# Kernel tuning notes

Measured on AMD Instinct MI355X. Metric: run time of the kernel, lower is better.

The kernel has to match this reference:

```python
import jax, jax.numpy as jnp
import numpy as np

N_NODES = 50000
N_EDGES = 800000
N_GRAPHS = 512
D_NODE = 64
D_EDGE = 32
Z_DIM = 2 * D_NODE + D_EDGE  # 160


def setup_inputs() -> dict:
    key = jax.random.key(0)
    ks = jax.random.split(key, 12)
    inp = {
        'x': jax.random.normal(ks[0], (N_NODES, D_NODE), dtype=jnp.float32),
        'edge_index': jax.random.randint(ks[1], (2, N_EDGES), 0, N_NODES, dtype=jnp.int64),
        'edge_attr': jax.random.uniform(ks[2], (N_EDGES, D_EDGE), dtype=jnp.float32),
        'batch': jnp.sort(jax.random.randint(ks[3], (N_NODES,), 0, N_GRAPHS, dtype=jnp.int64)),
        'Wf1': jax.random.normal(ks[4], (Z_DIM, D_NODE), dtype=jnp.float32) * 0.05,
        'bf1': jnp.zeros((D_NODE,), dtype=jnp.float32),
        'Ws1': jax.random.normal(ks[5], (Z_DIM, D_NODE), dtype=jnp.float32) * 0.05,
        'bs1': jnp.zeros((D_NODE,), dtype=jnp.float32),
        'Wf2': jax.random.normal(ks[6], (Z_DIM, D_NODE), dtype=jnp.float32) * 0.05,
        'bf2': jnp.zeros((D_NODE,), dtype=jnp.float32),
        'Ws2': jax.random.normal(ks[7], (Z_DIM, D_NODE), dtype=jnp.float32) * 0.05,
        'bs2': jnp.zeros((D_NODE,), dtype=jnp.float32),
        'W_out': jax.random.normal(ks[8], (D_NODE, 1), dtype=jnp.float32) * 0.05,
        'b_out': jnp.zeros((1,), dtype=jnp.float32),
    }
    return inp


def _cgconv(x, edge_index, edge_attr, Wf, bf, Ws, bs):
    # PyG CGConv: out_i = x_i + sum_{j in N(i)} sigmoid(lin_f(z_ij)) * softplus(lin_s(z_ij))
    # with z_ij = [x_i, x_j, e_ij]; source_to_target flow: j=edge_index[0], i=edge_index[1]
    src, dst = edge_index[0], edge_index[1]
    z = jnp.concatenate([x[dst], x[src], edge_attr], axis=-1)  # [E, 2d+dim]
    msg = jax.nn.sigmoid(z @ Wf + bf) * jax.nn.softplus(z @ Ws + bs)  # [E, d]
    aggr = jax.ops.segment_sum(msg, dst, num_segments=x.shape[0])
    return x + aggr


def reference(x, edge_index, edge_attr, batch, Wf1, bf1, Ws1, bs1, Wf2, bf2, Ws2, bs2, W_out, b_out):
    h = _cgconv(x, edge_index, edge_attr, Wf1, bf1, Ws1, bs1)
    h = _cgconv(h, edge_index, edge_attr, Wf2, bf2, Ws2, bs2)
    pooled = jax.ops.segment_sum(h, batch, num_segments=N_GRAPHS)  # global_add_pool [G, d]
    out = pooled @ W_out + b_out  # [G, 1]
    return out
```

## Files before the change

### kernel.cpp

```cpp
#include <hip/hip_runtime.h>
#include <math.h>

#define N_NODES 50000
#define N_EDGES 800000
#define N_GRAPHS 512
#define D 64
#define DE 32
#define NB_SCAN 196
#define NSTR 136
#define NB_SCAT 3125
#define NB_NT 1563
#define NB_FUSED 4689


typedef __attribute__((ext_vector_type(8))) short short8;
typedef __attribute__((ext_vector_type(4))) float floatx4;
union Frag { short8 s; unsigned u[4]; };
union U4   { uint4 v; unsigned u[4]; };

__device__ inline unsigned pk_bf16(float lo, float hi) {
    unsigned a = __float_as_uint(lo);
    unsigned b = __float_as_uint(hi);
    a = (a + 0x7FFFu + ((a >> 16) & 1u)) >> 16;
    b = (b + 0x7FFFu + ((b >> 16) & 1u)) >> 16;
    return a | (b << 16);
}
__device__ inline unsigned short bf16_1(float v) {
    unsigned a = __float_as_uint(v);
    return (unsigned short)((a + 0x7FFFu + ((a >> 16) & 1u)) >> 16);
}
__device__ inline float upk(unsigned u16) { return __uint_as_float(u16 << 16); }

__global__ __launch_bounds__(256) void hist_kernel(
    const int* __restrict__ ei, int* __restrict__ deg, int* __restrict__ rank)
{
    int e = blockIdx.x * 256 + threadIdx.x;
    rank[e] = atomicAdd(&deg[ei[N_EDGES + e]], 1);
}

__global__ __launch_bounds__(256) void scan1(
    const int* __restrict__ deg, int* __restrict__ off, int* __restrict__ tsum)
{
    __shared__ int s[256];
    int i = blockIdx.x * 256 + threadIdx.x;
    s[threadIdx.x] = (i < N_NODES) ? deg[i] : 0;
    __syncthreads();
    if (threadIdx.x == 0) {
        int run = 0;
        for (int k = 0; k < 256; ++k) { int t = s[k]; s[k] = run; run += t; }
        tsum[blockIdx.x] = run;
    }
    __syncthreads();
    if (i < N_NODES) off[i] = s[threadIdx.x];
}

__global__ __launch_bounds__(256) void scan2(int* __restrict__ tsum)
{
    __shared__ int s[256];
    int i = threadIdx.x;
    s[i] = (i < NB_SCAN) ? tsum[i] : 0;
    __syncthreads();
    if (i == 0) {
        int run = 0;
        for (int k = 0; k < NB_SCAN; ++k) { int t = s[k]; s[k] = run; run += t; }
    }
    __syncthreads();
    if (i < NB_SCAN) tsum[i] = s[i];
}

__global__ __launch_bounds__(256) void scan3(
    int* __restrict__ off, const int* __restrict__ tsum)
{
    int i = blockIdx.x * 256 + threadIdx.x;
    if (i < N_NODES) off[i] += tsum[blockIdx.x];
    if (i == N_NODES) off[i] = N_EDGES;
}

__global__ __launch_bounds__(256) void pack_W(
    const float* __restrict__ Wf1, const float* __restrict__ Ws1,
    const float* __restrict__ Wf2, const float* __restrict__ Ws2,
    uint4* __restrict__ WpkNT, uint4* __restrict__ WpkE)
{
    const int layer = blockIdx.y;
    const float* Wf = layer ? Wf2 : Wf1;
    const float* Ws = layer ? Ws2 : Ws1;
    const int i = blockIdx.x * 256 + threadIdx.x;
    if (i < 1024) {
        const int p    = i >> 9;
        const int cbi  = (i >> 6) & 7;
        const int l    = i & 63;
        const int n16  = l & 15, quad = l >> 4, kc = quad * 8;
        const int col  = cbi * 16 + n16;
        const int j    = col >> 1;
        const float* Wsel = (col & 1) ? Ws : Wf;
        const int rbase = p * 64;
        U4 b0, b1;
#pragma unroll
        for (int pp = 0; pp < 4; ++pp) {
            b0.u[pp] = pk_bf16(Wsel[(rbase + kc + 2 * pp) * 64 + j],
                               Wsel[(rbase + kc + 2 * pp + 1) * 64 + j]);
            b1.u[pp] = pk_bf16(Wsel[(rbase + 32 + kc + 2 * pp) * 64 + j],
                               Wsel[(rbase + 32 + kc + 2 * pp + 1) * 64 + j]);
        }
        uint4* o = WpkNT + ((size_t)layer * 1024 + i) * 2;
        o[0] = b0.v; o[1] = b1.v;
    } else if (i < 1280) {
        const int k  = i - 1024;
        const int jb = k >> 6;
        const int l  = k & 63;
        const int n16 = l & 15, quad = l >> 4, c0 = quad * 8;
        const int j = jb * 16 + n16;
        U4 bf_, bs_;
#pragma unroll
        for (int pp = 0; pp < 4; ++pp) {
            bf_.u[pp] = pk_bf16(Wf[(128 + c0 + 2 * pp) * 64 + j],
                                Wf[(128 + c0 + 2 * pp + 1) * 64 + j]);
            bs_.u[pp] = pk_bf16(Ws[(128 + c0 + 2 * pp) * 64 + j],
                                Ws[(128 + c0 + 2 * pp + 1) * 64 + j]);
        }
        uint4* o = WpkE + ((size_t)layer * 256 + k) * 2;
        o[0] = bf_.v; o[1] = bs_.v;
    }
}

__global__ __launch_bounds__(256) void fused_scatter_nt(
    const int* __restrict__ ei, const int* __restrict__ off,
    const int* __restrict__ rank, const float* __restrict__ ea,
    unsigned short* __restrict__ eaS, int2* __restrict__ sd_sorted,
    const float* __restrict__ H,
    const float* __restrict__ bf, const float* __restrict__ bs,
    const uint4* __restrict__ Wpk,
    unsigned short* __restrict__ Tdst, unsigned short* __restrict__ Tsrc,
    float* __restrict__ hinit)
{
    __shared__ unsigned short lt[4][16 * NSTR];
    const int k = blockIdx.x;

    if ((k % 3) != 2) {
        const int sid = k - (k / 3);
        if (sid >= NB_SCAT) return;
        int e = sid * 256 + threadIdx.x;
        int s = ei[e];
        int d = ei[N_EDGES + e];
        int pos = off[d] + rank[e];
        sd_sorted[pos] = make_int2(s, d);

        const float4* src4 = (const float4*)(ea + (size_t)e * 32);
        uint4* dst16 = (uint4*)(eaS + (size_t)pos * 32);
#pragma unroll
        for (int q = 0; q < 2; ++q) {
            float4 v0 = src4[4 * q + 0];
            float4 v1 = src4[4 * q + 1];
            float4 v2 = src4[4 * q + 2];
            float4 v3 = src4[4 * q + 3];
            uint4 o0;
            o0.x = pk_bf16(v0.x, v0.y); o0.y = pk_bf16(v0.z, v0.w);
            o0.z = pk_bf16(v1.x, v1.y); o0.w = pk_bf16(v1.z, v1.w);
            uint4 o1;
            o1.x = pk_bf16(v2.x, v2.y); o1.y = pk_bf16(v2.z, v2.w);
            o1.z = pk_bf16(v3.x, v3.y); o1.w = pk_bf16(v3.z, v3.w);
            dst16[2 * q + 0] = o0;
            dst16[2 * q + 1] = o1;
        }
        return;
    }

    const int lane = threadIdx.x & 63;
    const int wid  = threadIdx.x >> 6;
    const int n16  = lane & 15;
    const int quad = lane >> 4;
    const int kc   = quad * 8;
    unsigned short* L = lt[wid];

    const int gid = (k / 3) * 4 + wid;
    const int NW  = (N_NODES / 16) * 2;
    if (gid >= NW) return;
    const int ntile = gid >> 1;
    const int part  = gid & 1;
    unsigned short* Tout = part ? Tsrc : Tdst;

    const float* hrow = H + (size_t)(ntile * 16 + n16) * D;
    float4 q0 = *(const float4*)(hrow + kc);
    float4 q1 = *(const float4*)(hrow + kc + 4);
    float4 q2 = *(const float4*)(hrow + 32 + kc);
    float4 q3 = *(const float4*)(hrow + 32 + kc + 4);
    Frag a0, a1;
    a0.u[0] = pk_bf16(q0.x, q0.y); a0.u[1] = pk_bf16(q0.z, q0.w);
    a0.u[2] = pk_bf16(q1.x, q1.y); a0.u[3] = pk_bf16(q1.z, q1.w);
    a1.u[0] = pk_bf16(q2.x, q2.y); a1.u[1] = pk_bf16(q2.z, q2.w);
    a1.u[2] = pk_bf16(q3.x, q3.y); a1.u[3] = pk_bf16(q3.z, q3.w);

    if (part == 0) {
        float4* hp = (float4*)(hinit + (size_t)(ntile * 16 + n16) * D);
        hp[quad * 2]     = q0;
        hp[quad * 2 + 1] = q1;
        hp[8 + quad * 2] = q2;
        hp[9 + quad * 2] = q3;
    }

#pragma unroll
    for (int cbi = 0; cbi < 8; ++cbi) {
        const int col   = cbi * 16 + n16;
        const int sflag = col & 1;
        const int j     = col >> 1;

        Frag b0, b1;
        {
            const uint4* bp = Wpk + ((size_t)(part * 512 + cbi * 64 + lane)) * 2;
            *(uint4*)&b0 = bp[0];
            *(uint4*)&b1 = bp[1];
        }
        float bias = 0.0f;
        if (part == 0) bias = sflag ? bs[j] : bf[j];

        floatx4 acc = {bias, bias, bias, bias};
        acc = __builtin_amdgcn_mfma_f32_16x16x32_bf16(a0.s, b0.s, acc, 0, 0, 0);
        acc = __builtin_amdgcn_mfma_f32_16x16x32_bf16(a1.s, b1.s, acc, 0, 0, 0);

#pragma unroll
        for (int r = 0; r < 4; ++r)
            L[(quad * 4 + r) * NSTR + col] = bf16_1(acc[r]);
    }

#pragma unroll
    for (int it = 0; it < 4; ++it) {
        const int node_l = it * 4 + quad;
        const int c8     = n16 * 8;
        uint4 v = *(const uint4*)(L + node_l * NSTR + c8);
        *(uint4*)(Tout + (size_t)(ntile * 16 + node_l) * 128 + c8) = v;
    }
}

__global__ __launch_bounds__(256) void node_transform_mfma(
    const float* __restrict__ H,
    const float* __restrict__ bf,
    const float* __restrict__ bs,
    const uint4* __restrict__ Wpk,
    unsigned short* __restrict__ Tdst,
    unsigned short* __restrict__ Tsrc,
    float* __restrict__ hinit)
{
    __shared__ unsigned short lt[4][16 * NSTR];
    const int lane = threadIdx.x & 63;
    const int wid  = threadIdx.x >> 6;
    const int n16  = lane & 15;
    const int quad = lane >> 4;
    const int kc   = quad * 8;
    unsigned short* L = lt[wid];

    const int gid = blockIdx.x * 4 + wid;
    const int NW  = (N_NODES / 16) * 2;
    if (gid >= NW) return;
    const int ntile = gid >> 1;
    const int part  = gid & 1;
    unsigned short* Tout = part ? Tsrc : Tdst;

    const float* hrow = H + (size_t)(ntile * 16 + n16) * D;
    float4 q0 = *(const float4*)(hrow + kc);
    float4 q1 = *(const float4*)(hrow + kc + 4);
    float4 q2 = *(const float4*)(hrow + 32 + kc);
    float4 q3 = *(const float4*)(hrow + 32 + kc + 4);
    Frag a0, a1;
    a0.u[0] = pk_bf16(q0.x, q0.y); a0.u[1] = pk_bf16(q0.z, q0.w);
    a0.u[2] = pk_bf16(q1.x, q1.y); a0.u[3] = pk_bf16(q1.z, q1.w);
    a1.u[0] = pk_bf16(q2.x, q2.y); a1.u[1] = pk_bf16(q2.z, q2.w);
    a1.u[2] = pk_bf16(q3.x, q3.y); a1.u[3] = pk_bf16(q3.z, q3.w);

    if (part == 0) {
        float4* hp = (float4*)(hinit + (size_t)(ntile * 16 + n16) * D);
        hp[quad * 2]     = q0;
        hp[quad * 2 + 1] = q1;
        hp[8 + quad * 2] = q2;
        hp[9 + quad * 2] = q3;
    }

#pragma unroll
    for (int cbi = 0; cbi < 8; ++cbi) {
        const int col   = cbi * 16 + n16;
        const int sflag = col & 1;
        const int j     = col >> 1;

        Frag b0, b1;
        {
            const uint4* bp = Wpk + ((size_t)(part * 512 + cbi * 64 + lane)) * 2;
            *(uint4*)&b0 = bp[0];
            *(uint4*)&b1 = bp[1];
        }
        float bias = 0.0f;
        if (part == 0) bias = sflag ? bs[j] : bf[j];

        floatx4 acc = {bias, bias, bias, bias};
        acc = __builtin_amdgcn_mfma_f32_16x16x32_bf16(a0.s, b0.s, acc, 0, 0, 0);
        acc = __builtin_amdgcn_mfma_f32_16x16x32_bf16(a1.s, b1.s, acc, 0, 0, 0);

#pragma unroll
        for (int r = 0; r < 4; ++r)
            L[(quad * 4 + r) * NSTR + col] = bf16_1(acc[r]);
    }

#pragma unroll
    for (int it = 0; it < 4; ++it) {
        const int node_l = it * 4 + quad;
        const int c8     = n16 * 8;
        uint4 v = *(const uint4*)(L + node_l * NSTR + c8);
        *(uint4*)(Tout + (size_t)(ntile * 16 + node_l) * 128 + c8) = v;
    }
}

__global__ __launch_bounds__(256) void edge_message_mfma(
    const unsigned short* __restrict__ Tdst,
    const unsigned short* __restrict__ Tsrc,
    const unsigned short* __restrict__ eaS,
    const int2* __restrict__ sd_sorted,
    const uint4* __restrict__ WpkE,
    float* __restrict__ hout)
{
    const int lane = threadIdx.x & 63;
    const int wid  = threadIdx.x >> 6;
    const int n16  = lane & 15;
    const int quad = lane >> 4;
    const int c0   = quad * 8;

    Frag bfr[4], bsr[4];
#pragma unroll
    for (int jb = 0; jb < 4; ++jb) {
        *(uint4*)&bfr[jb] = WpkE[((size_t)(jb * 64 + lane)) * 2 + 0];
        *(uint4*)&bsr[jb] = WpkE[((size_t)(jb * 64 + lane)) * 2 + 1];
    }

    const int nwg = gridDim.x;
    const int xcd = blockIdx.x & 7;
    const int idx = blockIdx.x >> 3;
    const int q   = nwg >> 3, rr = nwg & 7;
    const int sb  = (xcd < rr ? xcd * (q + 1) : rr * (q + 1) + (xcd - rr) * q) + idx;
    const int w   = sb * 4 + wid;
    const int base = w * 64;

    const floatx4 zero = {0.0f, 0.0f, 0.0f, 0.0f};

    const int4* sdp4 = (const int4*)(sd_sorted + base + quad * 16);
    int4 sdq[8];
#pragma unroll
    for (int i = 0; i < 8; ++i) sdq[i] = sdp4[i];

#define SV(e) ((((e) & 1) != 0) ? sdq[(e) >> 1].z : sdq[(e) >> 1].x)
#define DV(e) ((((e) & 1) != 0) ? sdq[(e) >> 1].w : sdq[(e) >> 1].y)

    const unsigned short* aptr =
        eaS + (size_t)(base + (n16 >> 2) * 16 + (n16 & 3)) * 32 + c0;
    Frag af;
    af.s = *(const short8*)aptr;

    unsigned sbuf[2][4][4];
#pragma unroll
    for (int r = 0; r < 4; ++r) {
        const unsigned* srow = (const unsigned*)(Tsrc + (size_t)SV(r) * 128);
        sbuf[0][r][0] = srow[n16];
        sbuf[0][r][1] = srow[16 + n16];
        sbuf[0][r][2] = srow[32 + n16];
        sbuf[0][r][3] = srow[48 + n16];
    }

    int cur_d = -1;
    unsigned dr0 = 0, dr1 = 0, dr2 = 0, dr3 = 0;
    float acc0 = 0.f, acc1 = 0.f, acc2 = 0.f, acc3 = 0.f;

#pragma unroll
    for (int tt = 0; tt < 4; ++tt) {
        const int cb = tt & 1, nb = cb ^ 1;
        if (tt < 3) {
#pragma unroll
            for (int r = 0; r < 4; ++r) {
                const unsigned* srow =
                    (const unsigned*)(Tsrc + (size_t)SV(4 * (tt + 1) + r) * 128);
                sbuf[nb][r][0] = srow[n16];
                sbuf[nb][r][1] = srow[16 + n16];
                sbuf[nb][r][2] = srow[32 + n16];
                sbuf[nb][r][3] = srow[48 + n16];
            }
        }

        floatx4 accf[4], accs[4];
#pragma unroll
        for (int jb = 0; jb < 4; ++jb) {
            accf[jb] = __builtin_amdgcn_mfma_f32_16x16x32_bf16(af.s, bfr[jb].s, zero, 0, 0, 0);
            accs[jb] = __builtin_amdgcn_mfma_f32_16x16x32_bf16(af.s, bsr[jb].s, zero, 0, 0, 0);
        }
        if (tt < 3) af.s = *(const short8*)(aptr + (tt + 1) * 128);

#pragma unroll
        for (int r = 0; r < 4; ++r) {
            const int dv = DV(4 * tt + r);
            if (dv != cur_d) {
                if (cur_d >= 0) {
                    float* hp = hout + (size_t)cur_d * D + n16;
                    atomicAdd(hp +  0, acc0);
                    atomicAdd(hp + 16, acc1);
                    atomicAdd(hp + 32, acc2);
                    atomicAdd(hp + 48, acc3);
                }
                cur_d = dv;
                const unsigned* drow = (const unsigned*)(Tdst + (size_t)dv * 128);
                dr0 = drow[n16];
                dr1 = drow[16 + n16];
                dr2 = drow[32 + n16];
                dr3 = drow[48 + n16];
                acc0 = acc1 = acc2 = acc3 = 0.f;
            }
#pragma unroll
            for (int jb = 0; jb < 4; ++jb) {
                unsigned d2 = (jb == 0) ? dr0 : (jb == 1) ? dr1 : (jb == 2) ? dr2 : dr3;
                unsigned sv = sbuf[cb][r][jb];
                float vf = accf[jb][r] + upk(d2 & 0xFFFFu) + upk(sv & 0xFFFFu);
                float vs = accs[jb][r] + upk(d2 >> 16) + upk(sv >> 16);
                float sig = __builtin_amdgcn_rcpf(1.0f + __expf(-vf));
                float spl = fmaxf(vs, 0.0f) + __logf(1.0f + __expf(-fabsf(vs)));
                float msg = sig * spl;
                if      (jb == 0) acc0 += msg;
                else if (jb == 1) acc1 += msg;
                else if (jb == 2) acc2 += msg;
                else              acc3 += msg;
            }
        }
    }
#undef SV
#undef DV
    {
        float* hp = hout + (size_t)cur_d * D + n16;
        atomicAdd(hp +  0, acc0);
        atomicAdd(hp + 16, acc1);
        atomicAdd(hp + 32, acc2);
        atomicAdd(hp + 48, acc3);
    }
}

__global__ __launch_bounds__(256) void pool_kernel(
    const float* __restrict__ h,
    const int* __restrict__ batch,
    float* __restrict__ pooled)
{
    const int lane = threadIdx.x & 63;
    const int wid  = threadIdx.x >> 6;
    const int w = blockIdx.x * 4 + wid;
    const int n0 = w * 16;
    if (n0 >= N_NODES) return;
    const int nend = (n0 + 16 < N_NODES) ? (n0 + 16) : N_NODES;

    int cur = batch[n0];
    float acc = 0.0f;
    for (int n = n0; n < nend; ++n) {
        int b = batch[n];
        float v = h[(size_t)n * D + lane];
        if (b != cur) {
            atomicAdd(&pooled[(size_t)cur * D + lane], acc);
            cur = b; acc = v;
        } else {
            acc += v;
        }
    }
    atomicAdd(&pooled[(size_t)cur * D + lane], acc);
}

__global__ __launch_bounds__(256) void out_kernel(
    const float* __restrict__ pooled,
    const float* __restrict__ Wout,
    const float* __restrict__ bout,
    float* __restrict__ out)
{
    const int g = blockIdx.x * blockDim.x + threadIdx.x;
    if (g >= N_GRAPHS) return;
    float acc = bout[0];
#pragma unroll
    for (int j = 0; j < D; ++j) acc = fmaf(pooled[(size_t)g * D + j], Wout[j], acc);
    out[g] = acc;
}

extern "C" void kernel_launch(void* const* d_in, const int* in_sizes, int n_in,
                              void* d_out, int out_size, void* d_ws, size_t ws_size,
                              hipStream_t stream) {
    const float* x     = (const float*)d_in[0];
    const int*   ei    = (const int*)  d_in[1];
    const float* ea    = (const float*)d_in[2];
    const int*   batch = (const int*)  d_in[3];
    const float* Wf1   = (const float*)d_in[4];
    const float* bf1   = (const float*)d_in[5];
    const float* Ws1   = (const float*)d_in[6];
    const float* bs1   = (const float*)d_in[7];
    const float* Wf2   = (const float*)d_in[8];
    const float* bf2   = (const float*)d_in[9];
    const float* Ws2   = (const float*)d_in[10];
    const float* bs2   = (const float*)d_in[11];
    const float* Wout  = (const float*)d_in[12];
    const float* bout  = (const float*)d_in[13];
    float* out = (float*)d_out;

    char* base = (char*)d_ws;
    size_t o = 0;
    unsigned short* Tdst = (unsigned short*)(base + o); o += (size_t)N_NODES * 128 * 2;
    unsigned short* Tsrc = (unsigned short*)(base + o); o += (size_t)N_NODES * 128 * 2;
    unsigned short* eaS  = (unsigned short*)(base + o); o += (size_t)N_EDGES * 32 * 2;
    float* h1     = (float*)(base + o); o += (size_t)N_NODES * D * 4;
    float* h2     = (float*)(base + o); o += (size_t)N_NODES * D * 4;
    float* pooled = (float*)(base + o); o += (size_t)N_GRAPHS * D * 4;
    int* deg  = (int*)(base + o); o += (size_t)N_NODES * 4;
    int* off  = (int*)(base + o); o += (size_t)(N_NODES + 1) * 4;
    int* tsum = (int*)(base + o); o += 256 * 4;
    int2* sd_sorted = (int2*)(base + o); o += (size_t)N_EDGES * 8;
    uint4* WpkNT = (uint4*)(base + o); o += (size_t)2 * 1024 * 2 * 16;
    uint4* WpkE  = (uint4*)(base + o); o += (size_t)2 * 256 * 2 * 16;
    int* rank = (int*)h2;

    pack_W<<<dim3(5, 2), 256, 0, stream>>>(Wf1, Ws1, Wf2, Ws2, WpkNT, WpkE);

    hipMemsetAsync(deg, 0, (size_t)N_NODES * 4, stream);
    hist_kernel<<<N_EDGES / 256, 256, 0, stream>>>(ei, deg, rank);
    scan1<<<NB_SCAN, 256, 0, stream>>>(deg, off, tsum);
    scan2<<<1, 256, 0, stream>>>(tsum);
    scan3<<<NB_SCAN, 256, 0, stream>>>(off, tsum);

    fused_scatter_nt<<<NB_FUSED, 256, 0, stream>>>(
        ei, off, rank, ea, eaS, sd_sorted,
        x, bf1, bs1, WpkNT, Tdst, Tsrc, h1);

    edge_message_mfma<<<3125, 256, 0, stream>>>(Tdst, Tsrc, eaS, sd_sorted,
                                                WpkE, h1);

    node_transform_mfma<<<1563, 256, 0, stream>>>(h1, bf2, bs2, WpkNT + 2048, Tdst, Tsrc, h2);
    edge_message_mfma<<<3125, 256, 0, stream>>>(Tdst, Tsrc, eaS, sd_sorted,
                                                WpkE + 512, h2);

    hipMemsetAsync(pooled, 0, (size_t)N_GRAPHS * D * 4, stream);
    pool_kernel<<<782, 256, 0, stream>>>(h2, batch, pooled);
    out_kernel<<<2, 256, 0, stream>>>(pooled, Wout, bout, out);
}
```

Before: 446.5 us.

## Accumulate global pool incrementally via linearity and drop h2 and pool kernel

Uses linearity of the add-pool to build pooled from x plus each layer's scattered messages, adding atomics to pooled inside the edge message kernel and never materialising h2. Merges memsets and weight packing into one setup kernel, fuses the histogram with pooling of x, and merges scan2/scan3 into one kernel. This removes a full node-feature write/read and several launches, at the cost of extra contended atomics on the small pooled buffer.

Measured after the change: 840.5 us. +88.2%, slower.

```diff
diff --git a/kernel.cpp b/kernel.cpp
--- a/kernel.cpp
+++ b/kernel.cpp
@@ -9,7 +9,7 @@
 #define NB_SCAN 196
 #define NSTR 136
 #define NB_SCAT 3125
-#define NB_NT 1563
+#define NB_POOLX 782
 #define NB_FUSED 4689
 
 
@@ -31,60 +31,27 @@
 }
 __device__ inline float upk(unsigned u16) { return __uint_as_float(u16 << 16); }
 
-__global__ __launch_bounds__(256) void hist_kernel(
-    const int* __restrict__ ei, int* __restrict__ deg, int* __restrict__ rank)
-{
-    int e = blockIdx.x * 256 + threadIdx.x;
-    rank[e] = atomicAdd(&deg[ei[N_EDGES + e]], 1);
-}
-
-__global__ __launch_bounds__(256) void scan1(
-    const int* __restrict__ deg, int* __restrict__ off, int* __restrict__ tsum)
-{
-    __shared__ int s[256];
-    int i = blockIdx.x * 256 + threadIdx.x;
-    s[threadIdx.x] = (i < N_NODES) ? deg[i] : 0;
-    __syncthreads();
-    if (threadIdx.x == 0) {
-        int run = 0;
-        for (int k = 0; k < 256; ++k) { int t = s[k]; s[k] = run; run += t; }
-        tsum[blockIdx.x] = run;
-    }
-    __syncthreads();
-    if (i < N_NODES) off[i] = s[threadIdx.x];
-}
-
-__global__ __launch_bounds__(256) void scan2(int* __restrict__ tsum)
-{
-    __shared__ int s[256];
-    int i = threadIdx.x;
-    s[i] = (i < NB_SCAN) ? tsum[i] : 0;
-    __syncthreads();
-    if (i == 0) {
-        int run = 0;
-        for (int k = 0; k < NB_SCAN; ++k) { int t = s[k]; s[k] = run; run += t; }
-    }
-    __syncthreads();
-    if (i < NB_SCAN) tsum[i] = s[i];
-}
-
-__global__ __launch_bounds__(256) void scan3(
-    int* __restrict__ off, const int* __restrict__ tsum)
-{
-    int i = blockIdx.x * 256 + threadIdx.x;
-    if (i < N_NODES) off[i] += tsum[blockIdx.x];
-    if (i == N_NODES) off[i] = N_EDGES;
-}
-
-__global__ __launch_bounds__(256) void pack_W(
+__global__ __launch_bounds__(256) void setup_kernel(
     const float* __restrict__ Wf1, const float* __restrict__ Ws1,
     const float* __restrict__ Wf2, const float* __restrict__ Ws2,
-    uint4* __restrict__ WpkNT, uint4* __restrict__ WpkE)
-{
-    const int layer = blockIdx.y;
+    uint4* __restrict__ WpkNT, uint4* __restrict__ WpkE,
+    int* __restrict__ deg, float* __restrict__ pooled)
+{
+    const int b = blockIdx.x;
+    if (b >= 206) {
+        int i = (b - 206) * 256 + threadIdx.x;
+        if (i < N_GRAPHS * D) pooled[i] = 0.0f;
+        return;
+    }
+    if (b >= 10) {
+        int i = (b - 10) * 256 + threadIdx.x;
+        if (i < N_NODES) deg[i] = 0;
+        return;
+    }
+    const int layer = b / 5;
     const float* Wf = layer ? Wf2 : Wf1;
     const float* Ws = layer ? Ws2 : Ws1;
-    const int i = blockIdx.x * 256 + threadIdx.x;
+    const int i = (b % 5) * 256 + threadIdx.x;
     if (i < 1024) {
         const int p    = i >> 9;
         const int cbi  = (i >> 6) & 7;
@@ -121,6 +88,70 @@
         uint4* o = WpkE + ((size_t)layer * 256 + k) * 2;
         o[0] = bf_.v; o[1] = bs_.v;
     }
+}
+
+__global__ __launch_bounds__(256) void hist_pool(
+    const int* __restrict__ ei, int* __restrict__ deg, int* __restrict__ rank,
+    const float* __restrict__ x, const int* __restrict__ batch,
+    float* __restrict__ pooled)
+{
+    const int b = blockIdx.x;
+    if (b < NB_SCAT) {
+        int e = b * 256 + threadIdx.x;
+        rank[e] = atomicAdd(&deg[ei[N_EDGES + e]], 1);
+        return;
+    }
+    const int lane = threadIdx.x & 63;
+    const int wid  = threadIdx.x >> 6;
+    const int w = (b - NB_SCAT) * 4 + wid;
+    const int n0 = w * 16;
+    if (n0 >= N_NODES) return;
+    const int nend = (n0 + 16 < N_NODES) ? (n0 + 16) : N_NODES;
+
+    int cur = batch[n0];
+    float acc = 0.0f;
+    for (int n = n0; n < nend; ++n) {
+        int bb = batch[n];
+        float v = x[(size_t)n * D + lane];
+        if (bb != cur) {
+            atomicAdd(&pooled[(size_t)cur * D + lane], acc);
+            cur = bb; acc = v;
+        } else {
+            acc += v;
+        }
+    }
+    atomicAdd(&pooled[(size_t)cur * D + lane], acc);
+}
+
+__global__ __launch_bounds__(256) void scan1(
+    const int* __restrict__ deg, int* __restrict__ off, int* __restrict__ tsum)
+{
+    __shared__ int s[256];
+    int i = blockIdx.x * 256 + threadIdx.x;
+    s[threadIdx.x] = (i < N_NODES) ? deg[i] : 0;
+    __syncthreads();
+    if (threadIdx.x == 0) {
+        int run = 0;
+        for (int k = 0; k < 256; ++k) { int t = s[k]; s[k] = run; run += t; }
+        tsum[blockIdx.x] = run;
+    }
+    __syncthreads();
+    if (i < N_NODES) off[i] = s[threadIdx.x];
+}
+
+__global__ __launch_bounds__(256) void scan23(
+    int* __restrict__ off, const int* __restrict__ tsum)
+{
+    __shared__ int pfx;
+    if (threadIdx.x == 0) {
+        int run = 0;
+        for (int k = 0; k < (int)blockIdx.x; ++k) run += tsum[k];
+        pfx = run;
+    }
+    __syncthreads();
+    int i = blockIdx.x * 256 + threadIdx.x;
+    if (i < N_NODES) off[i] += pfx;
+    if (i == N_NODES) off[i] = N_EDGES;
 }
 
 __global__ __launch_bounds__(256) void fused_scatter_nt(
@@ -266,7 +297,7 @@
     a1.u[0] = pk_bf16(q2.x, q2.y); a1.u[1] = pk_bf16(q2.z, q2.w);
     a1.u[2] = pk_bf16(q3.x, q3.y); a1.u[3] = pk_bf16(q3.z, q3.w);
 
-    if (part == 0) {
+    if (hinit != nullptr && part == 0) {
         float4* hp = (float4*)(hinit + (size_t)(ntile * 16 + n16) * D);
         hp[quad * 2]     = q0;
         hp[quad * 2 + 1] = q1;
@@ -313,6 +344,8 @@
     const unsigned short* __restrict__ eaS,
     const int2* __restrict__ sd_sorted,
     const uint4* __restrict__ WpkE,
+    const int* __restrict__ batch,
+    float* __restrict__ pooled,
     float* __restrict__ hout)
 {
     const int lane = threadIdx.x & 63;
@@ -393,11 +426,19 @@
             const int dv = DV(4 * tt + r);
             if (dv != cur_d) {
                 if (cur_d >= 0) {
-                    float* hp = hout + (size_t)cur_d * D + n16;
-                    atomicAdd(hp +  0, acc0);
-                    atomicAdd(hp + 16, acc1);
-                    atomicAdd(hp + 32, acc2);
-                    atomicAdd(hp + 48, acc3);
+                    if (hout != nullptr) {
+                        float* hp = hout + (size_t)cur_d * D + n16;
+                        atomicAdd(hp +  0, acc0);
+                        atomicAdd(hp + 16, acc1);
+                        atomicAdd(hp + 32, acc2);
+                        atomicAdd(hp + 48, acc3);
+                    }
+                    const int bg = batch[cur_d];
+                    float* pp = pooled + (size_t)bg * D + n16;
+                    atomicAdd(pp +  0, acc0);
+                    atomicAdd(pp + 16, acc1);
+                    atomicAdd(pp + 32, acc2);
+                    atomicAdd(pp + 48, acc3);
                 }
                 cur_d = dv;
                 const unsigned* drow = (const unsigned*)(Tdst + (size_t)dv * 128);
@@ -426,39 +467,20 @@
 #undef SV
 #undef DV
     {
-        float* hp = hout + (size_t)cur_d * D + n16;
-        atomicAdd(hp +  0, acc0);
-        atomicAdd(hp + 16, acc1);
-        atomicAdd(hp + 32, acc2);
-        atomicAdd(hp + 48, acc3);
-    }
-}
-
-__global__ __launch_bounds__(256) void pool_kernel(
-    const float* __restrict__ h,
-    const int* __restrict__ batch,
-    float* __restrict__ pooled)
-{
-    const int lane = threadIdx.x & 63;
-    const int wid  = threadIdx.x >> 6;
-    const int w = blockIdx.x * 4 + wid;
-    const int n0 = w * 16;
-    if (n0 >= N_NODES) return;
-    const int nend = (n0 + 16 < N_NODES) ? (n0 + 16) : N_NODES;
-
-    int cur = batch[n0];
-    float acc = 0.0f;
-    for (int n = n0; n < nend; ++n) {
-        int b = batch[n];
-        float v = h[(size_t)n * D + lane];
-        if (b != cur) {
-            atomicAdd(&pooled[(size_t)cur * D + lane], acc);
-            cur = b; acc = v;
-        } else {
-            acc += v;
-        }
-    }
-    atomicAdd(&pooled[(size_t)cur * D + lane], acc);
+        if (hout != nullptr) {
+            float* hp = hout + (size_t)cur_d * D + n16;
+            atomicAdd(hp +  0, acc0);
+            atomicAdd(hp + 16, acc1);
+            atomicAdd(hp + 32, acc2);
+            atomicAdd(hp + 48, acc3);
+        }
+        const int bg = batch[cur_d];
+        float* pp = pooled + (size_t)bg * D + n16;
+        atomicAdd(pp +  0, acc0);
+        atomicAdd(pp + 16, acc1);
+        atomicAdd(pp + 32, acc2);
+        atomicAdd(pp + 48, acc3);
+    }
 }
 
 __global__ __launch_bounds__(256) void out_kernel(
@@ -500,36 +522,30 @@
     unsigned short* Tsrc = (unsigned short*)(base + o); o += (size_t)N_NODES * 128 * 2;
     unsigned short* eaS  = (unsigned short*)(base + o); o += (size_t)N_EDGES * 32 * 2;
     float* h1     = (float*)(base + o); o += (size_t)N_NODES * D * 4;
-    float* h2     = (float*)(base + o); o += (size_t)N_NODES * D * 4;
     float* pooled = (float*)(base + o); o += (size_t)N_GRAPHS * D * 4;
     int* deg  = (int*)(base + o); o += (size_t)N_NODES * 4;
     int* off  = (int*)(base + o); o += (size_t)(N_NODES + 1) * 4;
     int* tsum = (int*)(base + o); o += 256 * 4;
     int2* sd_sorted = (int2*)(base + o); o += (size_t)N_EDGES * 8;
+    int* rank = (int*)(base + o); o += (size_t)N_EDGES * 4;
     uint4* WpkNT = (uint4*)(base + o); o += (size_t)2 * 1024 * 2 * 16;
     uint4* WpkE  = (uint4*)(base + o); o += (size_t)2 * 256 * 2 * 16;
-    int* rank = (int*)h2;
-
-    pack_W<<<dim3(5, 2), 256, 0, stream>>>(Wf1, Ws1, Wf2, Ws2, WpkNT, WpkE);
-
-    hipMemsetAsync(deg, 0, (size_t)N_NODES * 4, stream);
-    hist_kernel<<<N_EDGES / 256, 256, 0, stream>>>(ei, deg, rank);
+
+    setup_kernel<<<334, 256, 0, stream>>>(Wf1, Ws1, Wf2, Ws2,
+                                          WpkNT, WpkE, deg, pooled);
+    hist_pool<<<NB_SCAT + NB_POOLX, 256, 0, stream>>>(ei, deg, rank,
+                                                      x, batch, pooled);
     scan1<<<NB_SCAN, 256, 0, stream>>>(deg, off, tsum);
-    scan2<<<1, 256, 0, stream>>>(tsum);
-    scan3<<<NB_SCAN, 256, 0, stream>>>(off, tsum);
-
+    scan23<<<NB_SCAN, 256, 0, stream>>>(off, tsum);
     fused_scatter_nt<<<NB_FUSED, 256, 0, stream>>>(
         ei, off, rank, ea, eaS, sd_sorted,
         x, bf1, bs1, WpkNT, Tdst, Tsrc, h1);
-
     edge_message_mfma<<<3125, 256, 0, stream>>>(Tdst, Tsrc, eaS, sd_sorted,
-                                                WpkE, h1);
-
-    node_transform_mfma<<<1563, 256, 0, stream>>>(h1, bf2, bs2, WpkNT + 2048, Tdst, Tsrc, h2);
+                                                WpkE, batch, pooled, h1);
+    node_transform_mfma<<<1563, 256, 0, stream>>>(h1, bf2, bs2, WpkNT + 2048,
+                                                  Tdst, Tsrc, nullptr);
     edge_message_mfma<<<3125, 256, 0, stream>>>(Tdst, Tsrc, eaS, sd_sorted,
-                                                WpkE + 512, h2);
-
-    hipMemsetAsync(pooled, 0, (size_t)N_GRAPHS * D * 4, stream);
-    pool_kernel<<<782, 256, 0, stream>>>(h2, batch, pooled);
+                                                WpkE + 512, batch, pooled,
+                                                nullptr);
     out_kernel<<<2, 256, 0, stream>>>(pooled, Wout, bout, out);
 }
```
